# Optimization experiments

Hardware: AMD Instinct MI355X
Metric: run time of the kernel (lower is better)

## Reference

```python
import jax, jax.numpy as jnp
import numpy as np

B, N, F_IN, F, C, E = 8192, 68, 2, 128, 16, 272
EPS = 1e-15


def graph_conv(x, src, dst, W_rel, W_root, b):
    # PyG GraphConv (aggr='add'): out_i = W_rel @ sum_{j->i} x_j + W_root @ x_i + b
    agg = jnp.zeros(x.shape, x.dtype).at[:, dst].add(x[:, src])  # [B,N,Fin]
    return agg @ W_rel.T + x @ W_root.T + b


def setup_inputs() -> dict:
    key = jax.random.key(0)
    ks = jax.random.split(key, 12)
    x = jax.random.normal(ks[0], (B, N, F_IN), jnp.float32)
    edge_index = jax.random.randint(ks[1], (2, E), 0, N, jnp.int32)
    adj = jax.random.uniform(ks[2], (B, N, N), jnp.float32)
    s = jax.random.normal(ks[3], (B, N, C), jnp.float32)
    pos = jax.random.normal(ks[4], (B, N, F_IN), jnp.float32)
    sc = 0.1
    W1_rel = jax.random.normal(ks[5], (F, F_IN), jnp.float32) * sc
    W1_root = jax.random.normal(ks[6], (F, F_IN), jnp.float32) * sc
    b1 = jnp.zeros((F,), jnp.float32)
    W2_rel = jax.random.normal(ks[7], (F, F), jnp.float32) * sc
    W2_root = jax.random.normal(ks[8], (F, F), jnp.float32) * sc
    b2 = jnp.zeros((F,), jnp.float32)
    W3_rel = jax.random.normal(ks[9], (F, F), jnp.float32) * sc
    W3_root = jax.random.normal(ks[10], (F, F), jnp.float32) * sc
    b3 = jnp.zeros((F,), jnp.float32)
    return dict(x=x, edge_index=edge_index, adj=adj, s=s, pos=pos,
                W1_rel=W1_rel, W1_root=W1_root, b1=b1,
                W2_rel=W2_rel, W2_root=W2_root, b2=b2,
                W3_rel=W3_rel, W3_root=W3_root, b3=b3)


def reference(x, edge_index, adj, s, pos,
              W1_rel, W1_root, b1, W2_rel, W2_root, b2, W3_rel, W3_root, b3):
    src, dst = edge_index[0], edge_index[1]
    h = jax.nn.relu(graph_conv(x, src, dst, W1_rel, W1_root, b1))
    h = jax.nn.relu(graph_conv(h, src, dst, W2_rel, W2_root, b2))
    h = jax.nn.relu(graph_conv(h, src, dst, W3_rel, W3_root, b3))  # [B,N,F]
    # dense_diff_pool
    s_sm = jax.nn.softmax(s, axis=-1)                       # [B,N,C]
    out = jnp.einsum('bnc,bnf->bcf', s_sm, h)               # [B,C,F]
    out_adj = jnp.einsum('bnc,bnm,bmk->bck', s_sm, adj, s_sm)  # [B,C,C]
    diff = adj - jnp.einsum('bnc,bmc->bnm', s_sm, s_sm)
    link_loss = jnp.sqrt(jnp.sum(diff * diff)) / adj.size
    ent_loss = jnp.mean(jnp.sum(-s_sm * jnp.log(s_sm + EPS), axis=-1))
    return (out, out_adj, link_loss, ent_loss, pos)
```

## Files before the change

kernel.cpp:

```cpp
#include <hip/hip_runtime.h>
#include <math.h>

#define B_   8192
#define N_   68
#define FIN  2
#define F_   128
#define C_   16
#define E_   272

#define OUT_OFF  0
#define ADJ_OFF  (B_*C_*F_)
#define LINK_IDX (ADJ_OFF + B_*C_*C_)
#define ENT_IDX  (LINK_IDX + 1)
#define POS_OFF  (ENT_IDX + 1)

#define WS_CSR_OFF  131072
#define WS_W_OFF    133120
#define WS_AG_OFF   264192

typedef __attribute__((ext_vector_type(8))) short bf16x8;
typedef __attribute__((ext_vector_type(4))) float f32x4;

#define SWZ256(r, cb) (((r) * 256) + ((cb) ^ (((r) & 7) << 4)))
#define SWZ512(r, cb) (((r) * 512) + ((cb) ^ (((r) & 7) << 4)))
#define SWZH(r, cb)   (((r) * 192) + ((cb) ^ (((r) & 3) << 4)))
#define MFMA16(a, bb, c) __builtin_amdgcn_mfma_f32_16x16x32_bf16((a), (bb), (c), 0, 0, 0)

__device__ __forceinline__ short bf16_rne(float x) {
  unsigned u = __builtin_bit_cast(unsigned, x);
  u += 0x7FFFu + ((u >> 16) & 1u);
  return (short)(u >> 16);
}
__device__ __forceinline__ short4 pack4(f32x4 v) {
  short4 s;
  s.x = bf16_rne(v[0]); s.y = bf16_rne(v[1]); s.z = bf16_rne(v[2]); s.w = bf16_rne(v[3]);
  return s;
}

__global__ void prep_kernel(const int* __restrict__ edge_index,
                            const float* __restrict__ W2r, const float* __restrict__ W2o,
                            const float* __restrict__ W3r, const float* __restrict__ W3o,
                            int* __restrict__ csr, short* __restrict__ wcat,
                            short* __restrict__ agw) {
  int gid = blockIdx.x * blockDim.x + threadIdx.x;
  for (int e = gid; e < 2 * F_ * 256; e += gridDim.x * blockDim.x) {
    int layer = e >> 15, idx = e & 32767;
    int j = idx >> 8, k = idx & 255;
    const float* Wr = layer ? W3r : W2r;
    const float* Wo = layer ? W3o : W2o;
    float v = (k < F_) ? Wr[j * F_ + k] : Wo[j * F_ + (k - F_)];
    wcat[e] = bf16_rne(v);
  }
  __shared__ unsigned short cnt[80 * 128];
  __shared__ int src_s[E_], dst_s[E_], cc[N_], offs[N_ + 1];
  if (blockIdx.x == 0) {
    int t = threadIdx.x;
    for (int i = t; i < 80 * 128; i += blockDim.x) cnt[i] = 0;
    for (int e = t; e < E_; e += blockDim.x) { src_s[e] = edge_index[e]; dst_s[e] = edge_index[E_ + e]; }
    for (int n = t; n < N_; n += blockDim.x) cc[n] = 0;
    __syncthreads();
    if (t == 0) {
      for (int e = 0; e < E_; ++e) { cnt[dst_s[e] * 128 + src_s[e]]++; cc[dst_s[e]]++; }
      offs[0] = 0;
      for (int n = 0; n < N_; ++n) offs[n + 1] = offs[n] + cc[n];
      for (int n = 0; n < N_; ++n) cc[n] = offs[n];
      for (int e = 0; e < E_; ++e) { int d = dst_s[e]; csr[N_ + 1 + cc[d]++] = src_s[e]; }
      for (int n = 0; n <= N_; ++n) csr[n] = offs[n];
    }
    __syncthreads();
    for (int i = t; i < 80 * 128; i += blockDim.x) agw[i] = bf16_rne((float)cnt[i]);
  }
}

__device__ __forceinline__ void layer_mfma(short* Hn, short* UT,
    const short* __restrict__ wl, const float* __restrict__ bias,
    const short* __restrict__ agw,
    int hinB, int houtB, int outT, int l15, int lg, int j0)
{
  bf16x8 Ar[4], Ao[4];
#pragma unroll
  for (int ks = 0; ks < 4; ++ks) {
    Ar[ks] = *(const bf16x8*)(wl + (j0 + l15) * 256 + ks * 32 + 8 * lg);
    Ao[ks] = *(const bf16x8*)(wl + (j0 + l15) * 256 + 128 + ks * 32 + 8 * lg);
  }
  f32x4 U0 = {0,0,0,0}, U1 = {0,0,0,0}, U2 = {0,0,0,0}, U3 = {0,0,0,0}, U4 = {0,0,0,0};
  f32x4 V0 = {0,0,0,0}, V1 = {0,0,0,0}, V2 = {0,0,0,0}, V3 = {0,0,0,0}, V4 = {0,0,0,0};
#define G1_(UN, VN, NT) do { \
  _Pragma("unroll") \
  for (int ks = 0; ks < 4; ++ks) { \
    bf16x8 b_ = *(const bf16x8*)((const char*)Hn + SWZ512((NT) * 16 + l15, hinB + ks * 64 + 16 * lg)); \
    UN = MFMA16(Ar[ks], b_, UN); \
    VN = MFMA16(Ao[ks], b_, VN); \
  } \
} while (0)
  G1_(U0, V0, 0); G1_(U1, V1, 1); G1_(U2, V2, 2); G1_(U3, V3, 3); G1_(U4, V4, 4);
#undef G1_
#define UTW_(UN, NT) do { \
  _Pragma("unroll") \
  for (int q = 0; q < 4; ++q) \
    *(short*)((char*)UT + SWZH(j0 + lg * 4 + q, ((NT) * 16 + l15) * 2)) = bf16_rne(UN[q]); \
} while (0)
  UTW_(U0, 0); UTW_(U1, 1); UTW_(U2, 2); UTW_(U3, 3); UTW_(U4, 4);
#undef UTW_
  bf16x8 aU[3];
#pragma unroll
  for (int ks = 0; ks < 3; ++ks)
    aU[ks] = *(const bf16x8*)((const char*)UT + SWZH(j0 + l15, ks * 64 + 16 * lg));
  float4 bv = *(const float4*)&bias[j0 + lg * 4];
#define G2_(VN, NT) do { \
  f32x4 acc = {0.f, 0.f, 0.f, 0.f}; \
  _Pragma("unroll") \
  for (int ks = 0; ks < 3; ++ks) \
    acc = MFMA16(aU[ks], *(const bf16x8*)(agw + ((NT) * 16 + l15) * 128 + ks * 32 + lg * 8), acc); \
  f32x4 v_; \
  v_[0] = fmaxf(acc[0] + VN[0] + bv.x, 0.f); \
  v_[1] = fmaxf(acc[1] + VN[1] + bv.y, 0.f); \
  v_[2] = fmaxf(acc[2] + VN[2] + bv.z, 0.f); \
  v_[3] = fmaxf(acc[3] + VN[3] + bv.w, 0.f); \
  if (!outT) { \
    *(short4*)((char*)Hn + SWZ512((NT) * 16 + l15, houtB + (j0 + lg * 4) * 2)) = pack4(v_); \
  } else { \
    _Pragma("unroll") \
    for (int q = 0; q < 4; ++q) \
      *(short*)((char*)UT + SWZH(j0 + lg * 4 + q, ((NT) * 16 + l15) * 2)) = bf16_rne(v_[q]); \
  } \
} while (0)
  G2_(V0, 0); G2_(V1, 1); G2_(V2, 2); G2_(V3, 3); G2_(V4, 4);
#undef G2_
}

__launch_bounds__(512, 4)
__global__ void layers_kernel(
    const float* __restrict__ x, const float* __restrict__ s,
    const float* __restrict__ W1r, const float* __restrict__ W1o, const float* __restrict__ b1,
    const float* __restrict__ b2f, const float* __restrict__ b3f,
    const short* __restrict__ wcat, const short* __restrict__ agw,
    float* __restrict__ out, const int* __restrict__ csr)
{
  __shared__ __align__(16) short Hn[80 * 256];
  __shared__ __align__(16) short UT[128 * 96];
  __shared__ __align__(16) short ssmT[16 * 128];
  __shared__ float xb[N_ * FIN], axb[N_ * FIN];
  __shared__ int offs[N_ + 1], srcs[E_];

  const int b = blockIdx.x, tid = threadIdx.x;
  const int lane = tid & 63, wave = tid >> 6;
  const int l15 = lane & 15, lg = lane >> 4;
  const int j0 = wave * 16;

  for (int i = tid; i < N_ + 1; i += 512) offs[i] = csr[i];
  for (int i = tid; i < E_; i += 512) srcs[i] = csr[N_ + 1 + i];
  for (int i = tid; i < N_ * FIN; i += 512) xb[i] = x[(size_t)b * N_ * FIN + i];
  {
    int4 zz; zz.x = 0; zz.y = 0; zz.z = 0; zz.w = 0;
    for (int i = tid; i < 384; i += 512) {
      int r = 68 + (i >> 5), cb = (i & 31) * 16;
      *(int4*)((char*)Hn + SWZ512(r, cb)) = zz;
    }
    long long z8 = 0;
    for (int i = tid; i < 128 * 2; i += 512) {
      int r = i >> 1, cb = 160 + (i & 1) * 16;
      *(int4*)((char*)UT + SWZH(r, cb)) = zz;
    }
    for (int i = tid; i < 16 * 7; i += 512) {
      int r = i / 7, cb = 136 + (i % 7) * 8;
      *(long long*)((char*)ssmT + SWZ256(r, cb)) = z8;
    }
  }
  if (tid < N_) {
    const float* srow = &s[((size_t)b * N_ + tid) * C_];
    float sv[16];
    float mx = -1e30f;
#pragma unroll
    for (int c = 0; c < 16; ++c) { sv[c] = srow[c]; mx = fmaxf(mx, sv[c]); }
    float sum = 0.f;
#pragma unroll
    for (int c = 0; c < 16; ++c) { sv[c] = expf(sv[c] - mx); sum += sv[c]; }
    float inv = 1.f / sum;
#pragma unroll
    for (int c = 0; c < 16; ++c)
      *(short*)((char*)ssmT + SWZ256(c, tid * 2)) = bf16_rne(sv[c] * inv);
  }
  __syncthreads();

  if (tid < N_) {
    float a0 = 0, a1 = 0;
    for (int e = offs[tid]; e < offs[tid + 1]; ++e) {
      int sr = srcs[e];
      a0 += xb[sr * 2]; a1 += xb[sr * 2 + 1];
    }
    axb[tid * 2] = a0; axb[tid * 2 + 1] = a1;
  }
  __syncthreads();

  {
    int f4 = (tid & 31) * 4;
    float4 R0 = *(const float4*)&W1r[f4 * 2], R1 = *(const float4*)&W1r[f4 * 2 + 4];
    float4 O0 = *(const float4*)&W1o[f4 * 2], O1 = *(const float4*)&W1o[f4 * 2 + 4];
    float4 Bv = *(const float4*)&b1[f4];
#pragma unroll
    for (int p = 0; p < 5; ++p) {
      int n = p * 16 + (tid >> 5);
      if (n < N_) {
        float a0 = axb[n * 2], a1 = axb[n * 2 + 1], x0 = xb[n * 2], x1 = xb[n * 2 + 1];
        f32x4 v;
        v[0] = fmaxf(a0 * R0.x + a1 * R0.y + x0 * O0.x + x1 * O0.y + Bv.x, 0.f);
        v[1] = fmaxf(a0 * R0.z + a1 * R0.w + x0 * O0.z + x1 * O0.w + Bv.y, 0.f);
        v[2] = fmaxf(a0 * R1.x + a1 * R1.y + x0 * O1.x + x1 * O1.y + Bv.z, 0.f);
        v[3] = fmaxf(a0 * R1.z + a1 * R1.w + x0 * O1.z + x1 * O1.w + Bv.w, 0.f);
        *(short4*)((char*)Hn + SWZ512(n, f4 * 2)) = pack4(v);
      }
    }
  }
  __syncthreads();

  layer_mfma(Hn, UT, wcat, b2f, agw, 0, 256, 0, l15, lg, j0);
  __syncthreads();

  layer_mfma(Hn, UT, wcat + 32768, b3f, agw, 256, 0, 1, l15, lg, j0);

  {
    f32x4 acc = {0.f, 0.f, 0.f, 0.f};
#pragma unroll
    for (int ks = 0; ks < 3; ++ks)
      acc = MFMA16(*(const bf16x8*)((const char*)UT + SWZH(j0 + l15, ks * 64 + 16 * lg)),
                   *(const bf16x8*)((const char*)ssmT + SWZ256(l15, ks * 64 + 16 * lg)), acc);
    float4 st; st.x = acc[0]; st.y = acc[1]; st.z = acc[2]; st.w = acc[3];
    *(float4*)&out[OUT_OFF + (size_t)b * C_ * F_ + l15 * F_ + j0 + lg * 4] = st;
  }
}

__launch_bounds__(512, 4)
__global__ void pool2_kernel(
    const float* __restrict__ adj, const float* __restrict__ s, const float* __restrict__ pos,
    float* __restrict__ out, double* __restrict__ partials)
{
  __shared__ __align__(16) short AdjA[80 * 128], AdjB2[80 * 128];
  __shared__ __align__(16) short ssmA[16 * 128], ssmB[16 * 128];
  __shared__ __align__(16) short TTA[16 * 128],  TTB[16 * 128];
  __shared__ double red[32];

  const int blk = blockIdx.x, tid = threadIdx.x;
  const int gA = blk * 2, gB = blk * 2 + 1;
  const int lane = tid & 63, wave = tid >> 6;
  const int l15 = lane & 15, lg = lane >> 4;

  {
    long long z8 = 0;
    for (int i = tid; i < 1200; i += 512) {
      int r = i / 15, cb = 136 + (i % 15) * 8;
      *(long long*)((char*)AdjA + SWZ256(r, cb)) = z8;
      *(long long*)((char*)AdjB2 + SWZ256(r, cb)) = z8;
    }
    for (int i = tid; i < 204; i += 512) {
      int r = 68 + i / 17, cb = (i % 17) * 8;
      *(long long*)((char*)AdjA + SWZ256(r, cb)) = z8;
      *(long long*)((char*)AdjB2 + SWZ256(r, cb)) = z8;
    }
    for (int i = tid; i < 112; i += 512) {
      int r = i / 7, cb = 136 + (i % 7) * 8;
      *(long long*)((char*)ssmA + SWZ256(r, cb)) = z8;
      *(long long*)((char*)ssmB + SWZ256(r, cb)) = z8;
      *(long long*)((char*)TTA + SWZ256(r, cb)) = z8;
      *(long long*)((char*)TTB + SWZ256(r, cb)) = z8;
    }
  }
  float sadjA = 0.f, sadjB = 0.f;
  const float* adjbA = &adj[(size_t)gA * N_ * N_];
  const float* adjbB = &adj[(size_t)gB * N_ * N_];
#pragma unroll
  for (int i = 0; i < 3; ++i) {
    int q4 = tid + 512 * i;
    if (q4 < 1156) {
      float4 vA = *(const float4*)&adjbA[q4 * 4];
      float4 vB = *(const float4*)&adjbB[q4 * 4];
      sadjA += vA.x * vA.x + vA.y * vA.y + vA.z * vA.z + vA.w * vA.w;
      sadjB += vB.x * vB.x + vB.y * vB.y + vB.z * vB.z + vB.w * vB.w;
      int n = q4 / 17, m4 = (q4 - n * 17) * 4;
      f32x4 fa; fa[0] = vA.x; fa[1] = vA.y; fa[2] = vA.z; fa[3] = vA.w;
      f32x4 fb; fb[0] = vB.x; fb[1] = vB.y; fb[2] = vB.z; fb[3] = vB.w;
      *(short4*)((char*)AdjA + SWZ256(n, m4 * 2)) = pack4(fa);
      *(short4*)((char*)AdjB2 + SWZ256(n, m4 * 2)) = pack4(fb);
    }
  }
  float entA = 0.f, entB = 0.f;
  {
    bool isA = (tid < N_);
    bool isB = (tid >= 128 && tid < 128 + N_);
    if (isA || isB) {
      int row = isB ? (tid - 128) : tid;
      const float* srow = &s[((size_t)(isB ? gB : gA) * N_ + row) * C_];
      short* ssmP = isB ? ssmB : ssmA;
      float sv[16], ev[16];
      float mx = -1e30f;
#pragma unroll
      for (int c = 0; c < 16; ++c) { sv[c] = srow[c]; mx = fmaxf(mx, sv[c]); }
      float sum = 0.f;
#pragma unroll
      for (int c = 0; c < 16; ++c) { ev[c] = expf(sv[c] - mx); sum += ev[c]; }
      float inv = 1.f / sum, ps = 0.f;
#pragma unroll
      for (int c = 0; c < 16; ++c) {
        float pv = ev[c] * inv;
        ps += pv * sv[c];
        *(short*)((char*)ssmP + SWZ256(c, row * 2)) = bf16_rne(pv);
      }
      float ent = (mx + logf(sum)) - ps;
      if (isB) entB = ent; else entA = ent;
    }
  }
  for (int i = tid; i < N_ * FIN; i += 512) {
    out[POS_OFF + (size_t)gA * N_ * FIN + i] = pos[(size_t)gA * N_ * FIN + i];
    out[POS_OFF + (size_t)gB * N_ * FIN + i] = pos[(size_t)gB * N_ * FIN + i];
  }
  __syncthreads();

  float g2A = 0.f, g2B = 0.f;
  if (wave < 5) {
    f32x4 accA = {0.f, 0.f, 0.f, 0.f};
    f32x4 accB = {0.f, 0.f, 0.f, 0.f};
#pragma unroll
    for (int ks = 0; ks < 3; ++ks) {
      accA = MFMA16(*(const bf16x8*)((const char*)AdjA + SWZ256(wave * 16 + l15, ks * 64 + 16 * lg)),
                    *(const bf16x8*)((const char*)ssmA + SWZ256(l15, ks * 64 + 16 * lg)), accA);
      accB = MFMA16(*(const bf16x8*)((const char*)AdjB2 + SWZ256(wave * 16 + l15, ks * 64 + 16 * lg)),
                    *(const bf16x8*)((const char*)ssmB + SWZ256(l15, ks * 64 + 16 * lg)), accB);
    }
#pragma unroll
    for (int r = 0; r < 4; ++r) {
      int n = wave * 16 + lg * 4 + r;
      if (n < N_) {
        *(short*)((char*)TTA + SWZ256(l15, n * 2)) = bf16_rne(accA[r]);
        *(short*)((char*)TTB + SWZ256(l15, n * 2)) = bf16_rne(accB[r]);
      }
    }
  } else if (wave == 5) {
    f32x4 accA = {0.f, 0.f, 0.f, 0.f};
    f32x4 accB = {0.f, 0.f, 0.f, 0.f};
#pragma unroll
    for (int ks = 0; ks < 3; ++ks) {
      bf16x8 a = *(const bf16x8*)((const char*)ssmA + SWZ256(l15, ks * 64 + 16 * lg));
      bf16x8 b = *(const bf16x8*)((const char*)ssmB + SWZ256(l15, ks * 64 + 16 * lg));
      accA = MFMA16(a, a, accA);
      accB = MFMA16(b, b, accB);
    }
#pragma unroll
    for (int r = 0; r < 4; ++r) { g2A += accA[r] * accA[r]; g2B += accB[r] * accB[r]; }
  }
  __syncthreads();

  float trA = 0.f, trB = 0.f;
  if (wave == 0) {
    f32x4 acc = {0.f, 0.f, 0.f, 0.f};
#pragma unroll
    for (int ks = 0; ks < 3; ++ks)
      acc = MFMA16(*(const bf16x8*)((const char*)ssmA + SWZ256(l15, ks * 64 + 16 * lg)),
                   *(const bf16x8*)((const char*)TTA + SWZ256(l15, ks * 64 + 16 * lg)), acc);
#pragma unroll
    for (int r = 0; r < 4; ++r) {
      int c = lg * 4 + r;
      out[ADJ_OFF + (size_t)gA * 256 + c * 16 + l15] = acc[r];
      if (c == l15) trA += acc[r];
    }
  } else if (wave == 1) {
    f32x4 acc = {0.f, 0.f, 0.f, 0.f};
#pragma unroll
    for (int ks = 0; ks < 3; ++ks)
      acc = MFMA16(*(const bf16x8*)((const char*)ssmB + SWZ256(l15, ks * 64 + 16 * lg)),
                   *(const bf16x8*)((const char*)TTB + SWZ256(l15, ks * 64 + 16 * lg)), acc);
#pragma unroll
    for (int r = 0; r < 4; ++r) {
      int c = lg * 4 + r;
      out[ADJ_OFF + (size_t)gB * 256 + c * 16 + l15] = acc[r];
      if (c == l15) trB += acc[r];
    }
  }

  double lkA = (double)sadjA - 2.0 * (double)trA + (double)g2A;
  double lkB = (double)sadjB - 2.0 * (double)trB + (double)g2B;
  double enA = (double)entA, enB = (double)entB;
  for (int o = 32; o > 0; o >>= 1) {
    lkA += __shfl_down(lkA, o); enA += __shfl_down(enA, o);
    lkB += __shfl_down(lkB, o); enB += __shfl_down(enB, o);
  }
  if ((tid & 63) == 0) {
    red[wave] = lkA; red[8 + wave] = enA;
    red[16 + wave] = lkB; red[24 + wave] = enB;
  }
  __syncthreads();
  if (tid == 0) {
    double LA = 0, EA = 0, LB = 0, EB = 0;
    for (int w = 0; w < 8; ++w) {
      LA += red[w]; EA += red[8 + w];
      LB += red[16 + w]; EB += red[24 + w];
    }
    partials[2 * gA] = LA; partials[2 * gA + 1] = EA;
    partials[2 * gB] = LB; partials[2 * gB + 1] = EB;
  }
}

__global__ void finalize_kernel(const double* __restrict__ partials, float* __restrict__ out) {
  __shared__ double red[16];
  int tid = threadIdx.x;
  double L = 0, En = 0;
  for (int i = tid; i < B_; i += 512) { L += partials[2 * i]; En += partials[2 * i + 1]; }
  for (int o = 32; o > 0; o >>= 1) { L += __shfl_down(L, o); En += __shfl_down(En, o); }
  if ((tid & 63) == 0) { red[tid >> 6] = L; red[8 + (tid >> 6)] = En; }
  __syncthreads();
  if (tid == 0) {
    double Ls = 0, Es = 0;
    for (int w = 0; w < 8; ++w) { Ls += red[w]; Es += red[8 + w]; }
    out[LINK_IDX] = (float)(sqrt(Ls) / (double)((size_t)B_ * N_ * N_));
    out[ENT_IDX] = (float)(Es / (double)((size_t)B_ * N_));
  }
}

extern "C" void kernel_launch(void* const* d_in, const int* in_sizes, int n_in,
                              void* d_out, int out_size, void* d_ws, size_t ws_size,
                              hipStream_t stream) {
  const float* x   = (const float*)d_in[0];
  const int*   ei  = (const int*)d_in[1];
  const float* adj = (const float*)d_in[2];
  const float* s   = (const float*)d_in[3];
  const float* pos = (const float*)d_in[4];
  const float* W1r = (const float*)d_in[5];
  const float* W1o = (const float*)d_in[6];
  const float* b1  = (const float*)d_in[7];
  const float* W2r = (const float*)d_in[8];
  const float* W2o = (const float*)d_in[9];
  const float* b2  = (const float*)d_in[10];
  const float* W3r = (const float*)d_in[11];
  const float* W3o = (const float*)d_in[12];
  const float* b3  = (const float*)d_in[13];

  float* out = (float*)d_out;
  double* partials = (double*)d_ws;
  int* csr = (int*)((char*)d_ws + WS_CSR_OFF);
  short* wcat = (short*)((char*)d_ws + WS_W_OFF);
  short* agw  = (short*)((char*)d_ws + WS_AG_OFF);

  prep_kernel<<<65, 512, 0, stream>>>(ei, W2r, W2o, W3r, W3o, csr, wcat, agw);
  layers_kernel<<<B_, 512, 0, stream>>>(x, s, W1r, W1o, b1, b2, b3, wcat, agw, out, csr);
  pool2_kernel<<<B_ / 2, 512, 0, stream>>>(adj, s, pos, out, partials);
  finalize_kernel<<<1, 512, 0, stream>>>(partials, out);
}
```

Baseline: 470.7 us.

## Halve layers_kernel LDS by overwriting H in place with a mid-layer barrier

Layer activations previously used a double-buffered H array in shared memory. Now a single 80x128 buffer is updated in place. A new barrier in the first layer, placed after the U-transpose reads and before the output writes, keeps the overwrite safe. Together with the launch bound raised from 4 to 6 blocks per CU, the smaller LDS footprint is meant to let more blocks run at once and hide latency. The cost is an extra barrier and tighter register limits, which could cause spills.

```diff
diff --git a/kernel.cpp b/kernel.cpp
--- a/kernel.cpp
+++ b/kernel.cpp
@@ -22,7 +22,6 @@
 typedef __attribute__((ext_vector_type(4))) float f32x4;
 
 #define SWZ256(r, cb) (((r) * 256) + ((cb) ^ (((r) & 7) << 4)))
-#define SWZ512(r, cb) (((r) * 512) + ((cb) ^ (((r) & 7) << 4)))
 #define SWZH(r, cb)   (((r) * 192) + ((cb) ^ (((r) & 3) << 4)))
 #define MFMA16(a, bb, c) __builtin_amdgcn_mfma_f32_16x16x32_bf16((a), (bb), (c), 0, 0, 0)
 
@@ -72,10 +71,10 @@
   }
 }
 
-__device__ __forceinline__ void layer_mfma(short* Hn, short* UT,
+__device__ __forceinline__ void layer_mfma(short* HnE, short* X,
     const short* __restrict__ wl, const float* __restrict__ bias,
     const short* __restrict__ agw,
-    int hinB, int houtB, int outT, int l15, int lg, int j0)
+    int outT, bool midBar, int l15, int lg, int j0)
 {
   bf16x8 Ar[4], Ao[4];
 #pragma unroll
@@ -88,7 +87,7 @@
 #define G1_(UN, VN, NT) do { \
   _Pragma("unroll") \
   for (int ks = 0; ks < 4; ++ks) { \
-    bf16x8 b_ = *(const bf16x8*)((const char*)Hn + SWZ512((NT) * 16 + l15, hinB + ks * 64 + 16 * lg)); \
+    bf16x8 b_ = *(const bf16x8*)((const char*)HnE + SWZ256((NT) * 16 + l15, ks * 64 + 16 * lg)); \
     UN = MFMA16(Ar[ks], b_, UN); \
     VN = MFMA16(Ao[ks], b_, VN); \
   } \
@@ -98,38 +97,38 @@
 #define UTW_(UN, NT) do { \
   _Pragma("unroll") \
   for (int q = 0; q < 4; ++q) \
-    *(short*)((char*)UT + SWZH(j0 + lg * 4 + q, ((NT) * 16 + l15) * 2)) = bf16_rne(UN[q]); \
+    *(short*)((char*)X + SWZH(j0 + lg * 4 + q, ((NT) * 16 + l15) * 2)) = bf16_rne(UN[q]); \
 } while (0)
   UTW_(U0, 0); UTW_(U1, 1); UTW_(U2, 2); UTW_(U3, 3); UTW_(U4, 4);
 #undef UTW_
-  bf16x8 aU[3];
-#pragma unroll
-  for (int ks = 0; ks < 3; ++ks)
-    aU[ks] = *(const bf16x8*)((const char*)UT + SWZH(j0 + l15, ks * 64 + 16 * lg));
+  bf16x8 aU0 = *(const bf16x8*)((const char*)X + SWZH(j0 + l15, 0 * 64 + 16 * lg));
+  bf16x8 aU1 = *(const bf16x8*)((const char*)X + SWZH(j0 + l15, 1 * 64 + 16 * lg));
+  bf16x8 aU2 = *(const bf16x8*)((const char*)X + SWZH(j0 + l15, 2 * 64 + 16 * lg));
+  if (midBar) __syncthreads();
   float4 bv = *(const float4*)&bias[j0 + lg * 4];
 #define G2_(VN, NT) do { \
   f32x4 acc = {0.f, 0.f, 0.f, 0.f}; \
-  _Pragma("unroll") \
-  for (int ks = 0; ks < 3; ++ks) \
-    acc = MFMA16(aU[ks], *(const bf16x8*)(agw + ((NT) * 16 + l15) * 128 + ks * 32 + lg * 8), acc); \
+  acc = MFMA16(aU0, *(const bf16x8*)(agw + ((NT) * 16 + l15) * 128 + 0 * 32 + lg * 8), acc); \
+  acc = MFMA16(aU1, *(const bf16x8*)(agw + ((NT) * 16 + l15) * 128 + 1 * 32 + lg * 8), acc); \
+  acc = MFMA16(aU2, *(const bf16x8*)(agw + ((NT) * 16 + l15) * 128 + 2 * 32 + lg * 8), acc); \
   f32x4 v_; \
   v_[0] = fmaxf(acc[0] + VN[0] + bv.x, 0.f); \
   v_[1] = fmaxf(acc[1] + VN[1] + bv.y, 0.f); \
   v_[2] = fmaxf(acc[2] + VN[2] + bv.z, 0.f); \
   v_[3] = fmaxf(acc[3] + VN[3] + bv.w, 0.f); \
   if (!outT) { \
-    *(short4*)((char*)Hn + SWZ512((NT) * 16 + l15, houtB + (j0 + lg * 4) * 2)) = pack4(v_); \
+    *(short4*)((char*)HnE + SWZ256((NT) * 16 + l15, (j0 + lg * 4) * 2)) = pack4(v_); \
   } else { \
     _Pragma("unroll") \
     for (int q = 0; q < 4; ++q) \
-      *(short*)((char*)UT + SWZH(j0 + lg * 4 + q, ((NT) * 16 + l15) * 2)) = bf16_rne(v_[q]); \
+      *(short*)((char*)X + SWZH(j0 + lg * 4 + q, ((NT) * 16 + l15) * 2)) = bf16_rne(v_[q]); \
   } \
 } while (0)
   G2_(V0, 0); G2_(V1, 1); G2_(V2, 2); G2_(V3, 3); G2_(V4, 4);
 #undef G2_
 }
 
-__launch_bounds__(512, 4)
+__launch_bounds__(512, 6)
 __global__ void layers_kernel(
     const float* __restrict__ x, const float* __restrict__ s,
     const float* __restrict__ W1r, const float* __restrict__ W1o, const float* __restrict__ b1,
@@ -137,8 +136,8 @@
     const short* __restrict__ wcat, const short* __restrict__ agw,
     float* __restrict__ out, const int* __restrict__ csr)
 {
-  __shared__ __align__(16) short Hn[80 * 256];
-  __shared__ __align__(16) short UT[128 * 96];
+  __shared__ __align__(16) short HnE[80 * 128];
+  __shared__ __align__(16) short X[128 * 96];
   __shared__ __align__(16) short ssmT[16 * 128];
   __shared__ float xb[N_ * FIN], axb[N_ * FIN];
   __shared__ int offs[N_ + 1], srcs[E_];
@@ -153,16 +152,16 @@
   for (int i = tid; i < N_ * FIN; i += 512) xb[i] = x[(size_t)b * N_ * FIN + i];
   {
     int4 zz; zz.x = 0; zz.y = 0; zz.z = 0; zz.w = 0;
-    for (int i = tid; i < 384; i += 512) {
-      int r = 68 + (i >> 5), cb = (i & 31) * 16;
-      *(int4*)((char*)Hn + SWZ512(r, cb)) = zz;
+    for (int i = tid; i < 192; i += 512) {
+      int r = 68 + (i >> 4), cb = (i & 15) * 16;
+      *(int4*)((char*)HnE + SWZ256(r, cb)) = zz;
+    }
+    for (int i = tid; i < 256; i += 512) {
+      int r = i >> 1, cb = 160 + (i & 1) * 16;
+      *(int4*)((char*)X + SWZH(r, cb)) = zz;
     }
     long long z8 = 0;
-    for (int i = tid; i < 128 * 2; i += 512) {
-      int r = i >> 1, cb = 160 + (i & 1) * 16;
-      *(int4*)((char*)UT + SWZH(r, cb)) = zz;
-    }
-    for (int i = tid; i < 16 * 7; i += 512) {
+    for (int i = tid; i < 112; i += 512) {
       int r = i / 7, cb = 136 + (i % 7) * 8;
       *(long long*)((char*)ssmT + SWZ256(r, cb)) = z8;
     }
@@ -208,22 +207,22 @@
         v[1] = fmaxf(a0 * R0.z + a1 * R0.w + x0 * O0.z + x1 * O0.w + Bv.y, 0.f);
         v[2] = fmaxf(a0 * R1.x + a1 * R1.y + x0 * O1.x + x1 * O1.y + Bv.z, 0.f);
         v[3] = fmaxf(a0 * R1.z + a1 * R1.w + x0 * O1.z + x1 * O1.w + Bv.w, 0.f);
-        *(short4*)((char*)Hn + SWZ512(n, f4 * 2)) = pack4(v);
+        *(short4*)((char*)HnE + SWZ256(n, f4 * 2)) = pack4(v);
       }
     }
   }
   __syncthreads();
 
-  layer_mfma(Hn, UT, wcat, b2f, agw, 0, 256, 0, l15, lg, j0);
-  __syncthreads();
-
-  layer_mfma(Hn, UT, wcat + 32768, b3f, agw, 256, 0, 1, l15, lg, j0);
+  layer_mfma(HnE, X, wcat, b2f, agw, 0, true, l15, lg, j0);
+  __syncthreads();
+
+  layer_mfma(HnE, X, wcat + 32768, b3f, agw, 1, false, l15, lg, j0);
 
   {
     f32x4 acc = {0.f, 0.f, 0.f, 0.f};
 #pragma unroll
     for (int ks = 0; ks < 3; ++ks)
-      acc = MFMA16(*(const bf16x8*)((const char*)UT + SWZH(j0 + l15, ks * 64 + 16 * lg)),
+      acc = MFMA16(*(const bf16x8*)((const char*)X + SWZH(j0 + l15, ks * 64 + 16 * lg)),
                    *(const bf16x8*)((const char*)ssmT + SWZ256(l15, ks * 64 + 16 * lg)), acc);
     float4 st; st.x = acc[0]; st.y = acc[1]; st.z = acc[2]; st.w = acc[3];
     *(float4*)&out[OUT_OFF + (size_t)b * C_ * F_ + l15 * F_ + j0 + lg * 4] = st;
```

Result: slower. 541.0 us (+14.9%).
